# Kernel optimization log

Measured on AMD Instinct MI355X. Metric: run time of the kernel, lower is better.

Reference implementation:

```python
import jax, jax.numpy as jnp
import numpy as np

MARGIN = 1.0


def _pairwise_sq_dist(emb):
    # squared euclidean distances, clamped at 0, diagonal zeroed (as in torch ref)
    ab = emb @ emb.T
    sq = jnp.diag(ab)
    d = jnp.maximum(sq[:, None] - 2.0 * ab + sq[None, :], 0.0)
    d = d * (d > 0.0).astype(d.dtype)  # error_mask step (faithful)
    B = d.shape[0]
    return d * (1.0 - jnp.eye(B, dtype=d.dtype))


def setup_inputs() -> dict:
    key = jax.random.key(0)
    k1, k2 = jax.random.split(key)
    emb = jax.random.normal(k1, (512, 256), dtype=jnp.float32)
    labels = jax.random.randint(k2, (512,), 0, 64, dtype=jnp.int64)
    return {"input": emb, "target": labels}


def reference(input, target):
    emb = input.astype(jnp.float32)
    pd = _pairwise_sq_dist(emb)                      # [B, B]
    B = pd.shape[0]
    adj = target[:, None] == target[None, :]         # [B, B]
    adj_not = ~adj

    # mask3[j, i, k]: negative k valid for anchor j w/ positive i (semi-hard: d(j,k) > d(j,i))
    mask3 = adj_not[:, None, :] & (pd[:, None, :] > pd[:, :, None])  # [B, B, B]

    # masked min over k: min of valid negatives, rowmax where masked out (torch trick equivalent)
    rowmax = pd.max(axis=1)                          # [B]
    negatives_outside = jnp.min(
        jnp.where(mask3, pd[:, None, :], rowmax[:, None, None]), axis=2
    )                                                # [B(anchor j), B(pos i)]

    # fallback: largest negative distance per anchor (masked max, rowmin where masked out)
    rowmin = pd.min(axis=1)                          # [B]
    negatives_inside = jnp.max(
        jnp.where(adj_not, pd, rowmin[:, None]), axis=1
    )                                                # [B]

    mask_final = jnp.any(mask3, axis=2)              # [B, B]
    semi_hard = jnp.where(mask_final, negatives_outside, negatives_inside[:, None])

    loss_mat = MARGIN + pd - semi_hard
    mask_pos = adj.astype(jnp.float32) - jnp.eye(B, dtype=jnp.float32)
    num_pos = mask_pos.sum()
    loss = jnp.maximum(loss_mat * mask_pos, 0.0).sum() / num_pos
    return loss.astype(input.dtype)
```

## Files before the change

### kernel.cpp

```cpp
#include <hip/hip_runtime.h>


#define BN 512
#define DF4 64

__device__ inline float wave_max64(float v){
  #pragma unroll
  for (int o = 32; o > 0; o >>= 1) v = fmaxf(v, __shfl_xor(v, o));
  return v;
}
__device__ inline float wave_min64(float v){
  #pragma unroll
  for (int o = 32; o > 0; o >>= 1) v = fminf(v, __shfl_xor(v, o));
  return v;
}

__global__ __launch_bounds__(256) void pd_gemm(
    const float* __restrict__ emb, float* __restrict__ pd, float* __restrict__ acc)
{
  __shared__ float As[32][260];
  __shared__ float Bs[32][260];
  __shared__ float sqA[32], sqB[32];
  __shared__ float outt[32][36];

  const int t  = threadIdx.x;
  const int bi = blockIdx.x & 15, bj = blockIdx.x >> 4;
  const int R0 = bi * 32, C0 = bj * 32;
  const float4* ef4 = reinterpret_cast<const float4*>(emb);

  if (blockIdx.x == 0 && t == 0){ acc[0] = 0.f; acc[1] = 0.f; ((int*)acc)[2] = 0; }

  #pragma unroll
  for (int j = 0; j < 8; ++j){
    int idx = t + j * 256;
    int r = idx >> 6, c = idx & 63;
    float4 va = ef4[(R0 + r) * DF4 + c];
    float4 vb = ef4[(C0 + r) * DF4 + c];
    *(float4*)&As[r][c * 4] = va;
    *(float4*)&Bs[r][c * 4] = vb;
  }
  {
    int half = t >> 7, u = t & 127;
    int r = u >> 2, part = u & 3;
    int base = ((half ? C0 : R0) + r) * DF4 + part * 16;
    float s = 0.f;
    #pragma unroll
    for (int i = 0; i < 16; ++i){
      float4 v = ef4[base + i];
      s += v.x*v.x + v.y*v.y + v.z*v.z + v.w*v.w;
    }
    s += __shfl_xor(s, 1); s += __shfl_xor(s, 2);
    if (part == 0){ if (half) sqB[r] = s; else sqA[r] = s; }
  }
  __syncthreads();

  const int r0 = t & 15, r1 = r0 + 16;
  const int c0 = t >> 4, c1 = c0 + 16;
  float a00 = 0.f, a01 = 0.f, a10 = 0.f, a11 = 0.f;
  #pragma unroll 8
  for (int kg = 0; kg < 64; ++kg){
    float4 A0 = *(const float4*)&As[r0][kg * 4];
    float4 A1 = *(const float4*)&As[r1][kg * 4];
    float4 B0 = *(const float4*)&Bs[c0][kg * 4];
    float4 B1 = *(const float4*)&Bs[c1][kg * 4];
    a00 += A0.x*B0.x + A0.y*B0.y + A0.z*B0.z + A0.w*B0.w;
    a01 += A0.x*B1.x + A0.y*B1.y + A0.z*B1.z + A0.w*B1.w;
    a10 += A1.x*B0.x + A1.y*B0.y + A1.z*B0.z + A1.w*B0.w;
    a11 += A1.x*B1.x + A1.y*B1.y + A1.z*B1.z + A1.w*B1.w;
  }

  const float sr0 = sqA[r0], sr1 = sqA[r1];
  const float sc0 = sqB[c0], sc1 = sqB[c1];
  float p00 = fmaxf(sr0 + sc0 - 2.f * a00, 0.f);
  float p01 = fmaxf(sr0 + sc1 - 2.f * a01, 0.f);
  float p10 = fmaxf(sr1 + sc0 - 2.f * a10, 0.f);
  float p11 = fmaxf(sr1 + sc1 - 2.f * a11, 0.f);
  if (bi == bj){
    if (r0 == c0) p00 = 0.f;
    if (r0 == c1) p01 = 0.f;
    if (r1 == c0) p10 = 0.f;
    if (r1 == c1) p11 = 0.f;
  }
  outt[r0][c0] = p00; outt[r0][c1] = p01;
  outt[r1][c0] = p10; outt[r1][c1] = p11;
  __syncthreads();

  int rr = t >> 3, cc = t & 7;
  float4 v = *(float4*)&outt[rr][cc * 4];
  *(float4*)&pd[(R0 + rr) * BN + C0 + cc * 4] = v;
}

__global__ __launch_bounds__(256) void mining(
    const float* __restrict__ pd, const int* __restrict__ labels,
    float* __restrict__ acc, float* __restrict__ out)
{
  __shared__ float wls[4], wcs[4];
  const int t = threadIdx.x, lane = t & 63, wid = t >> 6;
  const int j  = blockIdx.x * 4 + wid;
  const int lj = labels[j];

  const float4* prow = reinterpret_cast<const float4*>(pd + (size_t)j * BN);
  const int4*   lrow = reinterpret_cast<const int4*>(labels);
  float4 p0 = prow[lane * 2], p1 = prow[lane * 2 + 1];
  int4   l0 = lrow[lane * 2], l1 = lrow[lane * 2 + 1];
  float pk[8] = {p0.x, p0.y, p0.z, p0.w, p1.x, p1.y, p1.z, p1.w};
  int   lk[8] = {l0.x, l0.y, l0.z, l0.w, l1.x, l1.y, l1.z, l1.w};
  const int kbase = lane * 8;

  float ninside = 0.f;
  #pragma unroll
  for (int m = 0; m < 8; ++m)
    if (lk[m] != lj) ninside = fmaxf(ninside, pk[m]);
  ninside = wave_max64(ninside);

  float lsum = 0.f; int pcnt = 0;
  #pragma unroll
  for (int m = 0; m < 8; ++m){
    unsigned long long bal = __ballot(lk[m] == lj && (kbase + m) != j);
    while (bal){
      int L = (int)__ffsll((unsigned long long)bal) - 1;
      bal &= bal - 1;
      float tiv = __shfl(pk[m], L);
      float vmin = 3.402823466e38f;
      #pragma unroll
      for (int mm = 0; mm < 8; ++mm)
        if (lk[mm] != lj && pk[mm] > tiv) vmin = fminf(vmin, pk[mm]);
      vmin = wave_min64(vmin);
      float semi = (vmin < 3.0e38f) ? vmin : ninside;
      lsum += fmaxf(1.0f + tiv - semi, 0.f);
      ++pcnt;
    }
  }

  if (lane == 0){ wls[wid] = lsum; wcs[wid] = (float)pcnt; }
  __syncthreads();
  if (t == 0){
    float bl = wls[0] + wls[1] + wls[2] + wls[3];
    float bc = wcs[0] + wcs[1] + wcs[2] + wcs[3];
    atomicAdd(&acc[0], bl);
    atomicAdd(&acc[1], bc);
    __threadfence();
    int tk = atomicAdd((int*)acc + 2, 1);
    if (tk == 127){
      __threadfence();
      float tot = atomicAdd(&acc[0], 0.f);
      float cnt = atomicAdd(&acc[1], 0.f);
      out[0] = tot / cnt;
    }
  }
}

extern "C" void kernel_launch(void* const* d_in, const int* in_sizes, int n_in,
                              void* d_out, int out_size, void* d_ws, size_t ws_size,
                              hipStream_t stream) {
  const float* emb    = (const float*)d_in[0];
  const int*   labels = (const int*)d_in[1];
  float* out = (float*)d_out;
  float* pdw = (float*)d_ws;
  float* acc = pdw + BN * BN;
  pd_gemm<<<256, 256, 0, stream>>>(emb, pdw, acc);
  mining<<<128, 256, 0, stream>>>(pdw, labels, acc, out);
}
```

Baseline: 71.53 us.

## Split GEMM K dimension across waves with 4x4 register tiles and LDS atomic reduction

Reworks the pd_gemm inner loop so that each wave covers a quarter of the K dimension and each lane computes a 4x4 output tile. This raises register-level reuse of the shared-memory loads from 2x2 to 4x4. The four partial sums are then combined with shared-memory atomicAdd into a zeroed buffer, and the epilogue computes the distances and applies the diagonal zeroing. The cost is the LDS atomics, which may contend (4 waves per address), plus an extra zeroing pass.

```diff
diff --git a/kernel.cpp b/kernel.cpp
--- a/kernel.cpp
+++ b/kernel.cpp
@@ -14,30 +14,34 @@
   for (int o = 32; o > 0; o >>= 1) v = fminf(v, __shfl_xor(v, o));
   return v;
 }
+__device__ inline float dot4(float4 a, float4 b){
+  return a.x*b.x + a.y*b.y + a.z*b.z + a.w*b.w;
+}
 
 __global__ __launch_bounds__(256) void pd_gemm(
     const float* __restrict__ emb, float* __restrict__ pd, float* __restrict__ acc)
 {
   __shared__ float As[32][260];
   __shared__ float Bs[32][260];
+  __shared__ float pdbuf[32][36];
   __shared__ float sqA[32], sqB[32];
-  __shared__ float outt[32][36];
 
-  const int t  = threadIdx.x;
+  const int t    = threadIdx.x;
+  const int lane = t & 63, wid = t >> 6;
   const int bi = blockIdx.x & 15, bj = blockIdx.x >> 4;
   const int R0 = bi * 32, C0 = bj * 32;
   const float4* ef4 = reinterpret_cast<const float4*>(emb);
 
   if (blockIdx.x == 0 && t == 0){ acc[0] = 0.f; acc[1] = 0.f; ((int*)acc)[2] = 0; }
 
+  for (int idx = t; idx < 32 * 36; idx += 256) ((float*)pdbuf)[idx] = 0.f;
+
   #pragma unroll
   for (int j = 0; j < 8; ++j){
     int idx = t + j * 256;
     int r = idx >> 6, c = idx & 63;
-    float4 va = ef4[(R0 + r) * DF4 + c];
-    float4 vb = ef4[(C0 + r) * DF4 + c];
-    *(float4*)&As[r][c * 4] = va;
-    *(float4*)&Bs[r][c * 4] = vb;
+    *(float4*)&As[r][c * 4] = ef4[(R0 + r) * DF4 + c];
+    *(float4*)&Bs[r][c * 4] = ef4[(C0 + r) * DF4 + c];
   }
   {
     int half = t >> 7, u = t & 127;
@@ -54,40 +58,59 @@
   }
   __syncthreads();
 
-  const int r0 = t & 15, r1 = r0 + 16;
-  const int c0 = t >> 4, c1 = c0 + 16;
-  float a00 = 0.f, a01 = 0.f, a10 = 0.f, a11 = 0.f;
-  #pragma unroll 8
-  for (int kg = 0; kg < 64; ++kg){
-    float4 A0 = *(const float4*)&As[r0][kg * 4];
-    float4 A1 = *(const float4*)&As[r1][kg * 4];
-    float4 B0 = *(const float4*)&Bs[c0][kg * 4];
-    float4 B1 = *(const float4*)&Bs[c1][kg * 4];
-    a00 += A0.x*B0.x + A0.y*B0.y + A0.z*B0.z + A0.w*B0.w;
-    a01 += A0.x*B1.x + A0.y*B1.y + A0.z*B1.z + A0.w*B1.w;
-    a10 += A1.x*B0.x + A1.y*B0.y + A1.z*B0.z + A1.w*B0.w;
-    a11 += A1.x*B1.x + A1.y*B1.y + A1.z*B1.z + A1.w*B1.w;
+  const int a = lane >> 3, b = lane & 7;
+  float acc4[4][4];
+  #pragma unroll
+  for (int i = 0; i < 4; ++i)
+    #pragma unroll
+    for (int j = 0; j < 4; ++j) acc4[i][j] = 0.f;
+
+  const int kb = wid * 64;
+  #pragma unroll 4
+  for (int q = 0; q < 16; ++q){
+    const int kq = kb + q * 4;
+    float4 A0 = *(const float4*)&As[a     ][kq];
+    float4 A1 = *(const float4*)&As[a +  8][kq];
+    float4 A2 = *(const float4*)&As[a + 16][kq];
+    float4 A3 = *(const float4*)&As[a + 24][kq];
+    float4 B0 = *(const float4*)&Bs[b     ][kq];
+    float4 B1 = *(const float4*)&Bs[b +  8][kq];
+    float4 B2 = *(const float4*)&Bs[b + 16][kq];
+    float4 B3 = *(const float4*)&Bs[b + 24][kq];
+    acc4[0][0] += dot4(A0,B0); acc4[0][1] += dot4(A0,B1);
+    acc4[0][2] += dot4(A0,B2); acc4[0][3] += dot4(A0,B3);
+    acc4[1][0] += dot4(A1,B0); acc4[1][1] += dot4(A1,B1);
+    acc4[1][2] += dot4(A1,B2); acc4[1][3] += dot4(A1,B3);
+    acc4[2][0] += dot4(A2,B0); acc4[2][1] += dot4(A2,B1);
+    acc4[2][2] += dot4(A2,B2); acc4[2][3] += dot4(A2,B3);
+    acc4[3][0] += dot4(A3,B0); acc4[3][1] += dot4(A3,B1);
+    acc4[3][2] += dot4(A3,B2); acc4[3][3] += dot4(A3,B3);
   }
 
-  const float sr0 = sqA[r0], sr1 = sqA[r1];
-  const float sc0 = sqB[c0], sc1 = sqB[c1];
-  float p00 = fmaxf(sr0 + sc0 - 2.f * a00, 0.f);
-  float p01 = fmaxf(sr0 + sc1 - 2.f * a01, 0.f);
-  float p10 = fmaxf(sr1 + sc0 - 2.f * a10, 0.f);
-  float p11 = fmaxf(sr1 + sc1 - 2.f * a11, 0.f);
-  if (bi == bj){
-    if (r0 == c0) p00 = 0.f;
-    if (r0 == c1) p01 = 0.f;
-    if (r1 == c0) p10 = 0.f;
-    if (r1 == c1) p11 = 0.f;
-  }
-  outt[r0][c0] = p00; outt[r0][c1] = p01;
-  outt[r1][c0] = p10; outt[r1][c1] = p11;
+  #pragma unroll
+  for (int i = 0; i < 4; ++i)
+    #pragma unroll
+    for (int j = 0; j < 4; ++j)
+      atomicAdd(&pdbuf[a + 8 * i][b + 8 * j], acc4[i][j]);
   __syncthreads();
 
-  int rr = t >> 3, cc = t & 7;
-  float4 v = *(float4*)&outt[rr][cc * 4];
-  *(float4*)&pd[(R0 + rr) * BN + C0 + cc * 4] = v;
+  {
+    int r = t >> 3, cb = (t & 7) * 4;
+    float4 d = *(const float4*)&pdbuf[r][cb];
+    float sr = sqA[r];
+    float4 o;
+    o.x = fmaxf(sr + sqB[cb    ] - 2.f * d.x, 0.f);
+    o.y = fmaxf(sr + sqB[cb + 1] - 2.f * d.y, 0.f);
+    o.z = fmaxf(sr + sqB[cb + 2] - 2.f * d.z, 0.f);
+    o.w = fmaxf(sr + sqB[cb + 3] - 2.f * d.w, 0.f);
+    if (bi == bj){
+      if (r == cb    ) o.x = 0.f;
+      if (r == cb + 1) o.y = 0.f;
+      if (r == cb + 2) o.z = 0.f;
+      if (r == cb + 3) o.w = 0.f;
+    }
+    *(float4*)&pd[(size_t)(R0 + r) * BN + C0 + cb] = o;
+  }
 }
 
 __global__ __launch_bounds__(256) void mining(
```

Result: slower. 76.03 us (+6.3%).
